# Optimization experiments

Hardware: AMD Instinct MI355X
Metric: run time of the kernel (lower is better)

Reference implementation:

```python
import jax, jax.numpy as jnp
import numpy as np

# ---- constants from init_kwargs ----
TAU_MEM = 10.0
TAU_SYN = np.array([5.0, 2.0], dtype=np.float32)
THRESHOLD = 1.0
WINDOW = 0.3
BATCH = 32
T = 1024
N_NEURONS = 1024
N_SYN = len(TAU_SYN)

def _bitshift(tau):
    b = np.round(np.log2(np.asarray(tau, dtype=np.float32)))
    return np.maximum(b, 0.0).astype(np.float32)

DASH_MEM = float(_bitshift(TAU_MEM))          # 3.0 -> decay factor 2^-3
DASH_SYN = _bitshift(TAU_SYN)                  # [2.0, 1.0]
MEM_DECAY = np.float32(2.0 ** (-DASH_MEM))     # fraction removed per step
SYN_DECAY = (2.0 ** (-DASH_SYN)).astype(np.float32)  # (n_syn,)


def setup_inputs() -> dict:
    key = jax.random.key(0)
    # Bernoulli spike raster, (batch*T, n_syn, n_neurons)
    u = jax.random.uniform(key, (BATCH * T, N_SYN, N_NEURONS), dtype=jnp.float32)
    binary_input = (u < 0.2).astype(jnp.float32)
    return {"binary_input": binary_input}


def _lif_scan(syn_out):
    """syn_out: (T, B, N, n_syn). Bitshift-decay LIF with membrane-subtract reset."""
    syn_decay = jnp.asarray(SYN_DECAY)  # (n_syn,)
    mem_decay = jnp.float32(MEM_DECAY)
    vmem0 = jnp.zeros((BATCH, N_NEURONS), jnp.float32)
    isyn0 = jnp.zeros((BATCH, N_NEURONS, N_SYN), jnp.float32)

    def step(carry, inp_t):
        vmem, isyn = carry
        # bitshift decay: x -= x >> dash  <=>  x -= x * 2^-dash
        isyn = isyn - isyn * syn_decay + inp_t            # (B, N, n_syn)
        vmem = vmem - vmem * mem_decay + isyn.sum(-1)     # (B, N)
        spk = (vmem >= THRESHOLD).astype(vmem.dtype)
        vmem = vmem - spk * THRESHOLD                     # membrane subtract
        return (vmem, isyn), (spk, vmem)

    (_, _), (spikes, vmem_rec) = jax.lax.scan(step, (vmem0, isyn0), syn_out)
    return spikes, vmem_rec  # (T, B, N) each


def reference(binary_input):
    # (B*T, n_syn, N) -> (B, T, n_syn, N) -> (T, B, n_syn, N) -> (T, B, N, n_syn)
    x = binary_input.reshape(BATCH, T, N_SYN, N_NEURONS)
    x = jnp.swapaxes(x, 0, 1)
    x = jnp.moveaxis(x, -2, -1)
    spikes, _ = _lif_scan(x)
    # (T, B, N) -> (B, T, N) -> (B*T, N)
    out = jnp.swapaxes(spikes, 0, 1).reshape(BATCH * T, N_NEURONS)
    return out
```

## Files before the change

### kernel.cpp

```cpp
#include <hip/hip_runtime.h>


#define TT 1024
#define NN 1024
#define BB 32
#define UU 16

__global__ __launch_bounds__(64, 1)
void lif_scan_kernel(const float* __restrict__ in, float* __restrict__ out) {
    const int gid = blockIdx.x * 64 + threadIdx.x;
    const int b = gid >> 10;
    const int n = gid & (NN - 1);

    const float* __restrict__ ip = in + (size_t)b * TT * 2 * NN + n;
    float* __restrict__ op = out + (size_t)b * TT * NN + n;

    const float SD0 = 0.25f;
    const float SD1 = 0.5f;
    const float MD  = 0.125f;

    float i0 = 0.0f, i1 = 0.0f, v = 0.0f;

    float x0[UU], x1[UU];
#pragma unroll
    for (int j = 0; j < UU; ++j) {
        x0[j] = ip[j * 2048];
        x1[j] = ip[j * 2048 + 1024];
    }

    for (int tc = 0; tc < TT - UU; tc += UU) {
        float y0[UU], y1[UU];
        const float* pn = ip + (tc + UU) * 2048;
#pragma unroll
        for (int j = 0; j < UU; ++j) {
            y0[j] = pn[j * 2048];
            y1[j] = pn[j * 2048 + 1024];
        }
        float* po = op + tc * NN;
#pragma unroll
        for (int j = 0; j < UU; ++j) {
            i0 = (i0 - i0 * SD0) + x0[j];
            i1 = (i1 - i1 * SD1) + x1[j];
            float vd = v - v * MD;
            v = vd + (i0 + i1);
            float spk = (v >= 1.0f) ? 1.0f : 0.0f;
            v -= spk;
            po[j * NN] = spk;
        }
#pragma unroll
        for (int j = 0; j < UU; ++j) { x0[j] = y0[j]; x1[j] = y1[j]; }
    }

    {
        float* po = op + (TT - UU) * NN;
#pragma unroll
        for (int j = 0; j < UU; ++j) {
            i0 = (i0 - i0 * SD0) + x0[j];
            i1 = (i1 - i1 * SD1) + x1[j];
            float vd = v - v * MD;
            v = vd + (i0 + i1);
            float spk = (v >= 1.0f) ? 1.0f : 0.0f;
            v -= spk;
            po[j * NN] = spk;
        }
    }
}

extern "C" void kernel_launch(void* const* d_in, const int* in_sizes, int n_in,
                              void* d_out, int out_size, void* d_ws, size_t ws_size,
                              hipStream_t stream) {
    const float* in = (const float*)d_in[0];
    float* out = (float*)d_out;
    dim3 grid(BB * NN / 64);
    dim3 block(64);
    hipLaunchKernelGGL(lif_scan_kernel, grid, block, 0, stream, in, out);
}
```

Baseline: 390.5 us.

## Use four-stage register ring buffer to prefetch input chunks three ahead

Replaces the two-buffer prefetch (16 steps ahead) with a four-buffer rotating ring of 8-step chunks, keeping three chunks of loads in flight while computing the current one. This deepens memory-level parallelism for the latency-bound per-thread scan and removes the register copy between buffers. The loop is manually unrolled across buffers, and register pressure stays similar at 64 floats of prefetch.

```diff
diff --git a/kernel.cpp b/kernel.cpp
--- a/kernel.cpp
+++ b/kernel.cpp
@@ -4,7 +4,31 @@
 #define TT 1024
 #define NN 1024
 #define BB 32
-#define UU 16
+#define UU 8
+#define NCHUNK (TT / UU)
+
+#define LOADC(X0, X1, c) do {                                          \
+    const float* __restrict__ p_ = ip + (size_t)(c) * (UU * 2048);     \
+    _Pragma("unroll")                                                  \
+    for (int j_ = 0; j_ < UU; ++j_) {                                  \
+        X0[j_] = p_[j_ * 2048];                                        \
+        X1[j_] = p_[j_ * 2048 + 1024];                                 \
+    }                                                                  \
+} while (0)
+
+#define COMPC(X0, X1, c) do {                                          \
+    float* __restrict__ po_ = op + (size_t)(c) * (UU * NN);            \
+    _Pragma("unroll")                                                  \
+    for (int j_ = 0; j_ < UU; ++j_) {                                  \
+        i0 = (i0 - i0 * SD0) + X0[j_];                                 \
+        i1 = (i1 - i1 * SD1) + X1[j_];                                 \
+        float vd_ = v - v * MD;                                        \
+        v = vd_ + (i0 + i1);                                           \
+        float spk_ = (v >= 1.0f) ? 1.0f : 0.0f;                        \
+        v -= spk_;               \
+        po_[j_ * NN] = spk_;                                           \
+    }                                                                  \
+} while (0)
 
 __global__ __launch_bounds__(64, 1)
 void lif_scan_kernel(const float* __restrict__ in, float* __restrict__ out) {
@@ -21,49 +45,28 @@
 
     float i0 = 0.0f, i1 = 0.0f, v = 0.0f;
 
-    float x0[UU], x1[UU];
-#pragma unroll
-    for (int j = 0; j < UU; ++j) {
-        x0[j] = ip[j * 2048];
-        x1[j] = ip[j * 2048 + 1024];
+    float a0[UU], a1[UU];
+    float b0[UU], b1[UU];
+    float c0[UU], c1[UU];
+    float d0[UU], d1[UU];
+
+    LOADC(a0, a1, 0);
+    LOADC(b0, b1, 1);
+    LOADC(c0, c1, 2);
+
+    int c = 0;
+    for (int i = 0; i < (NCHUNK / 4) - 1; ++i, c += 4) {
+        LOADC(d0, d1, c + 3);  COMPC(a0, a1, c);
+        LOADC(a0, a1, c + 4);  COMPC(b0, b1, c + 1);
+        LOADC(b0, b1, c + 5);  COMPC(c0, c1, c + 2);
+        LOADC(c0, c1, c + 6);  COMPC(d0, d1, c + 3);
     }
 
-    for (int tc = 0; tc < TT - UU; tc += UU) {
-        float y0[UU], y1[UU];
-        const float* pn = ip + (tc + UU) * 2048;
-#pragma unroll
-        for (int j = 0; j < UU; ++j) {
-            y0[j] = pn[j * 2048];
-            y1[j] = pn[j * 2048 + 1024];
-        }
-        float* po = op + tc * NN;
-#pragma unroll
-        for (int j = 0; j < UU; ++j) {
-            i0 = (i0 - i0 * SD0) + x0[j];
-            i1 = (i1 - i1 * SD1) + x1[j];
-            float vd = v - v * MD;
-            v = vd + (i0 + i1);
-            float spk = (v >= 1.0f) ? 1.0f : 0.0f;
-            v -= spk;
-            po[j * NN] = spk;
-        }
-#pragma unroll
-        for (int j = 0; j < UU; ++j) { x0[j] = y0[j]; x1[j] = y1[j]; }
-    }
-
-    {
-        float* po = op + (TT - UU) * NN;
-#pragma unroll
-        for (int j = 0; j < UU; ++j) {
-            i0 = (i0 - i0 * SD0) + x0[j];
-            i1 = (i1 - i1 * SD1) + x1[j];
-            float vd = v - v * MD;
-            v = vd + (i0 + i1);
-            float spk = (v >= 1.0f) ? 1.0f : 0.0f;
-            v -= spk;
-            po[j * NN] = spk;
-        }
-    }
+    LOADC(d0, d1, NCHUNK - 1);
+    COMPC(a0, a1, NCHUNK - 4);
+    COMPC(b0, b1, NCHUNK - 3);
+    COMPC(c0, c1, NCHUNK - 2);
+    COMPC(d0, d1, NCHUNK - 1);
 }
 
 extern "C" void kernel_launch(void* const* d_in, const int* in_sizes, int n_in,
```

Measured after the change: 394.8 us. No clear change (+1.1%).
